# Optimization experiments

Hardware: AMD Instinct MI355X
Metric: run time of the kernel (lower is better)

The kernel has to match this reference:

```python
import jax, jax.numpy as jnp
import numpy as np

BN_EPS = 1e-5


def _interpolate(xyz1, xyz2, points2):
    # squared pairwise distances [B, N, S]
    d = (jnp.sum(xyz1 ** 2, -1)[:, :, None]
         + jnp.sum(xyz2 ** 2, -1)[:, None, :]
         - 2.0 * jnp.einsum('bnc,bsc->bns', xyz1, xyz2))
    # 3 smallest distances (torch does a full sort; top-3 is the same math)
    neg_d, idx = jax.lax.top_k(-d, 3)          # [B, N, 3]
    dists = -neg_d
    w = 1.0 / (dists + 1e-8)
    w = w / jnp.sum(w, -1, keepdims=True)
    # gather points2 features at idx: [B, N, 3, D]
    gathered = jnp.take_along_axis(points2[:, None, :, :],
                                   idx[:, :, :, None], axis=2)
    return jnp.sum(gathered * w[:, :, :, None], axis=2)  # [B, N, D]


def _conv_bn_relu(x, w, b, gamma, beta):
    # x: [B, N, Cin]; 1x1 Conv1d == per-point dense layer
    y = jnp.einsum('bnc,oc->bno', x, w) + b
    mean = jnp.mean(y, axis=(0, 1))
    var = jnp.mean((y - mean) ** 2, axis=(0, 1))  # biased var (torch BN training)
    y = (y - mean) * jax.lax.rsqrt(var + BN_EPS) * gamma + beta
    return jax.nn.relu(y)


def setup_inputs() -> dict:
    key = jax.random.key(0)
    ks = jax.random.split(key, 8)
    B, N, S, D1, D2 = 8, 8192, 2048, 128, 256
    in_ch, mlp = D1 + D2, [256, 128]
    inp = {
        'xyz1': jax.random.normal(ks[0], (B, N, 3), jnp.float32),
        'xyz2': jax.random.normal(ks[1], (B, S, 3), jnp.float32),
        'points1': jax.random.normal(ks[2], (B, N, D1), jnp.float32),
        'points2': jax.random.normal(ks[3], (B, S, D2), jnp.float32),
    }
    c = in_ch
    for i, o in enumerate(mlp):
        kw = jax.random.fold_in(ks[4], i)
        inp[f'w{i}'] = jax.random.normal(kw, (o, c), jnp.float32) * (1.0 / np.sqrt(c))
        inp[f'b{i}'] = jnp.zeros((o,), jnp.float32)
        inp[f'g{i}'] = jnp.ones((o,), jnp.float32)
        inp[f'beta{i}'] = jnp.zeros((o,), jnp.float32)
        c = o
    return inp


def reference(xyz1, xyz2, points1, points2,
              w0, b0, g0, beta0, w1, b1, g1, beta1):
    interp = _interpolate(xyz1, xyz2, points2)          # [B, N, D2]
    x = jnp.concatenate([points1, interp], axis=-1)     # [B, N, D1+D2]
    x = _conv_bn_relu(x, w0, b0, g0, beta0)
    x = _conv_bn_relu(x, w1, b1, g1, beta1)
    return x                                            # [B, N, mlp[-1]]
```

## Files before the change

### kernel.cpp

```cpp
#include <hip/hip_runtime.h>
#include <hip/hip_bf16.h>

#define BATCH 8
#define NPTS  8192
#define SPTS  2048
#define D1C   128
#define D2C   256
#define C_IN  384
#define O0    256
#define O1    128
#define MROWS (BATCH * NPTS)
#define NCHUNK 8
#define CHSZ   256

typedef __attribute__((ext_vector_type(8))) short short8v;
typedef __attribute__((ext_vector_type(4))) float f32x4;
typedef unsigned long long u64;

#define PKINIT 0x7FE0000000000000ULL

__device__ __forceinline__ unsigned short f2bf(float f) {
    union { float f; unsigned u; } v; v.f = f;
    unsigned u = v.u;
    return (unsigned short)((u + 0x7fffu + ((u >> 16) & 1u)) >> 16);
}
__device__ __forceinline__ float bf2f(unsigned short h) {
    union { unsigned u; float f; } v; v.u = ((unsigned)h) << 16;
    return v.f;
}
__device__ __forceinline__ void gload_lds16(const void* g, void* l) {
    __builtin_amdgcn_global_load_lds(
        (const __attribute__((address_space(1))) void*)g,
        (__attribute__((address_space(3))) void*)l, 16, 0, 0);
}

__device__ __forceinline__ double pack_di(float d, int idx) {
    union { float f; unsigned u; } b; b.f = d;
    unsigned db = b.u;
    unsigned u  = db ^ ((unsigned)((int)db >> 31) | 0x80000000u);
    union { u64 q; double x; } p;
    p.q = ((u64)u << 31) | (unsigned)idx;
    return p.x;
}
__device__ __forceinline__ void unpack_di(double x, float* d, int* idx) {
    union { double x; u64 q; } p; p.x = x;
    unsigned u = (unsigned)(p.q >> 31);
    unsigned db = (u & 0x80000000u) ? (u ^ 0x80000000u) : ~u;
    union { unsigned u; float f; } b; b.u = db;
    *d = b.f;
    *idx = (int)(p.q & 0x7FFu);
}
__device__ __forceinline__ void ins3(double& p0, double& p1, double& p2, double x) {
    double l0 = fmax(p0, x);
    p0 = fmin(p0, x);
    double l1 = fmax(p1, l0);
    p1 = fmin(p1, l0);
    p2 = fmin(p2, l1);
}

__global__ __launch_bounds__(256, 8) void nn3_scan(
    const float* __restrict__ xyz1, const float* __restrict__ xyz2,
    u64* __restrict__ candP)
{
    __shared__ float4 P[CHSZ];
    const int t  = threadIdx.x;
    const int qb = blockIdx.x;
    const int c  = blockIdx.y;
    const int b  = qb >> 5;

    {
        const float* src = xyz2 + ((size_t)b * SPTS + c * CHSZ) * 3;
        float px = src[t * 3 + 0];
        float py = src[t * 3 + 1];
        float pz = src[t * 3 + 2];
        P[t] = make_float4(px, py, pz, px * px + py * py + pz * pz);
    }
    __syncthreads();

    const int q = qb * 256 + t;
    const float* qp = xyz1 + (size_t)q * 3;
    const float qx = qp[0], qy = qp[1], qz = qp[2];
    const float qn = qx * qx + qy * qy + qz * qz;

    union { u64 q; double x; } init; init.q = PKINIT;
    double p0 = init.x, p1 = init.x, p2 = init.x;
    const int gbase = c * CHSZ;

    #pragma unroll 4
    for (int s = 0; s < CHSZ; ++s) {
        float4 p = P[s];
        float dot = qx * p.x + qy * p.y + qz * p.z;
        float d = (qn + p.w) - 2.0f * dot;
        ins3(p0, p1, p2, pack_di(d, gbase + s));
    }

    union { double x; u64 q; } o0, o1, o2;
    o0.x = p0; o1.x = p1; o2.x = p2;
    const size_t base = (size_t)c * (MROWS * 3) + (size_t)q * 3;
    candP[base + 0] = o0.q;
    candP[base + 1] = o1.q;
    candP[base + 2] = o2.q;
}

__global__ __launch_bounds__(256) void nn3_merge(
    const u64* __restrict__ candP,
    int* __restrict__ idx3, float* __restrict__ wgt3)
{
    const int q = blockIdx.x * 256 + threadIdx.x;

    union { u64 q; double x; } init; init.q = PKINIT;
    double p0 = init.x, p1 = init.x, p2 = init.x;

    #pragma unroll
    for (int c = 0; c < NCHUNK; ++c) {
        const size_t base = (size_t)c * (MROWS * 3) + (size_t)q * 3;
        #pragma unroll
        for (int j = 0; j < 3; ++j) {
            union { u64 q; double x; } v; v.q = candP[base + j];
            ins3(p0, p1, p2, v.x);
        }
    }

    float d0, d1, d2; int i0, i1, i2;
    unpack_di(p0, &d0, &i0);
    unpack_di(p1, &d1, &i1);
    unpack_di(p2, &d2, &i2);

    float wa = 1.0f / (d0 + 1e-8f);
    float wb = 1.0f / (d1 + 1e-8f);
    float wc = 1.0f / (d2 + 1e-8f);
    float inv = 1.0f / (wa + wb + wc);
    wa *= inv; wb *= inv; wc *= inv;

    idx3[q * 3 + 0] = i0;
    idx3[q * 3 + 1] = i1;
    idx3[q * 3 + 2] = i2;
    wgt3[q * 3 + 0] = wa;
    wgt3[q * 3 + 1] = wb;
    wgt3[q * 3 + 2] = wc;
}

__global__ __launch_bounds__(256) void cvt_weights(
    const float* __restrict__ w0, const float* __restrict__ w1,
    unsigned short* __restrict__ w0bf, unsigned short* __restrict__ w1bf)
{
    int i = blockIdx.x * 256 + threadIdx.x;
    const int n0 = O0 * C_IN / 4;
    const float* src; unsigned short* dst; int j;
    if (i < n0) { src = w0; dst = w0bf; j = i; }
    else        { src = w1; dst = w1bf; j = i - n0; }
    float4 v = ((const float4*)src)[j];
    ushort4 o;
    o.x = f2bf(v.x); o.y = f2bf(v.y); o.z = f2bf(v.z); o.w = f2bf(v.w);
    ((ushort4*)dst)[j] = o;
}

__global__ __launch_bounds__(256) void interp_kernel(
    const float* __restrict__ points2,
    const int* __restrict__ idx3, const float* __restrict__ wgt3,
    unsigned short* __restrict__ xI)
{
    const int w    = threadIdx.x >> 6;
    const int lane = threadIdx.x & 63;
    const int blk   = blockIdx.x;
    const int xcd   = blk & 7;
    const int local = blk >> 3;
    const int m     = (xcd * 2048 + local) * 4 + w;
    const int b     = xcd;

    const float* p2b = points2 + (size_t)b * SPTS * D2C;
    const int  gi0 = idx3[m * 3 + 0];
    const int  gi1 = idx3[m * 3 + 1];
    const int  gi2 = idx3[m * 3 + 2];
    const float w0 = wgt3[m * 3 + 0];
    const float w1 = wgt3[m * 3 + 1];
    const float w2 = wgt3[m * 3 + 2];

    float4 a  = *(const float4*)(p2b + (size_t)gi0 * D2C + lane * 4);
    float4 bb = *(const float4*)(p2b + (size_t)gi1 * D2C + lane * 4);
    float4 c  = *(const float4*)(p2b + (size_t)gi2 * D2C + lane * 4);

    ushort4 o;
    o.x = f2bf(w0 * a.x + w1 * bb.x + w2 * c.x);
    o.y = f2bf(w0 * a.y + w1 * bb.y + w2 * c.y);
    o.z = f2bf(w0 * a.z + w1 * bb.z + w2 * c.z);
    o.w = f2bf(w0 * a.w + w1 * bb.w + w2 * c.w);
    *(ushort4*)(xI + (size_t)m * D2C + lane * 4) = o;
}

__global__ __launch_bounds__(512, 4) void gemm0_mfma(
    const float* __restrict__ points1, const unsigned short* __restrict__ xI,
    const unsigned short* __restrict__ w0bf, const float* __restrict__ b0,
    unsigned short* __restrict__ y0bf,
    float* __restrict__ sum0, float* __restrict__ sq0)
{
    __shared__ __align__(16) unsigned short As[2][128 * 32];
    __shared__ __align__(16) unsigned short Bs[2][256 * 32];

    const int t    = threadIdx.x;
    const int lane = t & 63;
    const int w    = t >> 6;
    const int wm   = w >> 2;
    const int wn   = w & 3;
    const int rowBase = blockIdx.x * 128;

    const int r      = t >> 2;
    const int ks_log = (t & 3) ^ ((t >> 3) & 3);

    const float* p1row = points1 + (size_t)(rowBase + r) * D1C;
    const unsigned short* xrow = xI + (size_t)(rowBase + r) * D2C + ks_log * 8;
    const unsigned short* gB0 = w0bf + (size_t)r * C_IN + ks_log * 8;
    const unsigned short* gB1 = w0bf + (size_t)(128 + r) * C_IN + ks_log * 8;

    const int rp = (lane & 15) * 64 + (((lane >> 4) ^ ((lane >> 1) & 3)) * 16);

    f32x4 acc[4][4] = {};

    auto stage = [&](int buf, int kt) {
        gload_lds16(gB0 + kt * 32, (char*)Bs[buf] + w * 1024);
        gload_lds16(gB1 + kt * 32, (char*)Bs[buf] + 8192 + w * 1024);
        if (kt < 4) {
            const int k = kt * 32 + ks_log * 8;
            float4 f0 = *(const float4*)(p1row + k);
            float4 f1 = *(const float4*)(p1row + k + 4);
            short8v av;
            av[0] = (short)f2bf(f0.x); av[1] = (short)f2bf(f0.y);
            av[2] = (short)f2bf(f0.z); av[3] = (short)f2bf(f0.w);
            av[4] = (short)f2bf(f1.x); av[5] = (short)f2bf(f1.y);
            av[6] = (short)f2bf(f1.z); av[7] = (short)f2bf(f1.w);
            *(short8v*)(As[buf] + t * 8) = av;
        } else {
            gload_lds16(xrow + (kt - 4) * 32, (char*)As[buf] + w * 1024);
        }
    };

    auto compute = [&](int buf) {
        const char* aB = (const char*)As[buf] + (wm * 64) * 64 + rp;
        const char* bB = (const char*)Bs[buf] + (wn * 64) * 64 + rp;
        short8v a[4], bv[4];
        #pragma unroll
        for (int m = 0; m < 4; ++m) a[m]  = *(const short8v*)(aB + m * 1024);
        #pragma unroll
        for (int n = 0; n < 4; ++n) bv[n] = *(const short8v*)(bB + n * 1024);
        #pragma unroll
        for (int m = 0; m < 4; ++m)
            #pragma unroll
            for (int n = 0; n < 4; ++n)
                acc[m][n] = __builtin_amdgcn_mfma_f32_16x16x32_bf16(
                    a[m], bv[n], acc[m][n], 0, 0, 0);
    };

    stage(0, 0);
    __syncthreads();
    #pragma unroll
    for (int kt = 0; kt < C_IN / 32; ++kt) {
        if (kt + 1 < C_IN / 32) stage((kt + 1) & 1, kt + 1);
        compute(kt & 1);
        __syncthreads();
    }

    const int colw = wn * 64 + (lane & 15);
    const int rowE = rowBase + wm * 64 + ((lane >> 4) * 4);
    float bias[4];
    #pragma unroll
    for (int n = 0; n < 4; ++n) bias[n] = b0[colw + n * 16];

    float cs[4] = {0.f, 0.f, 0.f, 0.f}, cq[4] = {0.f, 0.f, 0.f, 0.f};
    #pragma unroll
    for (int m = 0; m < 4; ++m)
        #pragma unroll
        for (int n = 0; n < 4; ++n)
            #pragma unroll
            for (int j = 0; j < 4; ++j) {
                float v = acc[m][n][j] + bias[n];
                y0bf[(size_t)(rowE + m * 16 + j) * O0 + colw + n * 16] = f2bf(v);
                cs[n] += v; cq[n] += v * v;
            }

    #pragma unroll
    for (int n = 0; n < 4; ++n) {
        float s = cs[n], qv = cq[n];
        s  += __shfl_xor(s, 16);  s  += __shfl_xor(s, 32);
        qv += __shfl_xor(qv, 16); qv += __shfl_xor(qv, 32);
        if (lane < 16) {
            atomicAdd(&sum0[colw + n * 16], s);
            atomicAdd(&sq0[colw + n * 16], qv);
        }
    }
}

__global__ void stats_kernel(const float* __restrict__ sum, const float* __restrict__ sq,
                             const float* __restrict__ g, const float* __restrict__ beta,
                             float* __restrict__ scale, float* __restrict__ shift,
                             int C, float invM)
{
    int c = blockIdx.x * blockDim.x + threadIdx.x;
    if (c < C) {
        float mean = sum[c] * invM;
        float var  = sq[c] * invM - mean * mean;
        float s = g[c] * rsqrtf(var + 1e-5f);
        scale[c] = s;
        shift[c] = beta[c] - mean * s;
    }
}

__global__ __launch_bounds__(256, 2) void gemm1_mfma(
    const unsigned short* __restrict__ x1, const unsigned short* __restrict__ w1bf,
    const float* __restrict__ scale0, const float* __restrict__ shift0,
    const float* __restrict__ b1, unsigned short* __restrict__ y1bf,
    float* __restrict__ sum1, float* __restrict__ sq1)
{
    __shared__ __align__(16) unsigned short As[2][128 * 32];
    __shared__ __align__(16) unsigned short Bs[2][128 * 32];
    __shared__ float sc[O0], sh[O0];

    const int t    = threadIdx.x;
    const int lane = t & 63;
    const int w    = t >> 6;
    const int wm   = w >> 1, wn = w & 1;
    const int rowBase = blockIdx.x * 128;

    sc[t] = scale0[t];
    sh[t] = shift0[t];
    __syncthreads();

    const int r      = t >> 2;
    const int kl     = t & 3;
    const int kp     = kl ^ ((r >> 1) & 3);
    const int ks_log = kl ^ ((r >> 1) & 3);

    const unsigned short* gA0 = x1 + (size_t)(rowBase + r) * O0 + kl * 8;
    const unsigned short* gA1 = x1 + (size_t)(rowBase + 64 + r) * O0 + kl * 8;
    const unsigned short* gB0 = w1bf + (size_t)r * O0 + ks_log * 8;
    const unsigned short* gB1 = w1bf + (size_t)(64 + r) * O0 + ks_log * 8;

    const int rp = (lane & 15) * 64 + (((lane >> 4) ^ ((lane >> 1) & 3)) * 16);

    f32x4 acc[4][4] = {};

    auto stage = [&](int buf, int kt) {
        gload_lds16(gB0 + kt * 32, (char*)Bs[buf] + w * 1024);
        gload_lds16(gB1 + kt * 32, (char*)Bs[buf] + 4096 + w * 1024);

        const int ch = kt * 32 + kl * 8;
        float4 s0v = *(const float4*)(sc + ch);
        float4 s1v = *(const float4*)(sc + ch + 4);
        float4 h0v = *(const float4*)(sh + ch);
        float4 h1v = *(const float4*)(sh + ch + 4);
        short8v v0 = *(const short8v*)(gA0 + kt * 32);
        short8v v1 = *(const short8v*)(gA1 + kt * 32);
        short8v o0, o1;
        o0[0] = (short)f2bf(fmaxf(0.f, bf2f((unsigned short)v0[0]) * s0v.x + h0v.x));
        o0[1] = (short)f2bf(fmaxf(0.f, bf2f((unsigned short)v0[1]) * s0v.y + h0v.y));
        o0[2] = (short)f2bf(fmaxf(0.f, bf2f((unsigned short)v0[2]) * s0v.z + h0v.z));
        o0[3] = (short)f2bf(fmaxf(0.f, bf2f((unsigned short)v0[3]) * s0v.w + h0v.w));
        o0[4] = (short)f2bf(fmaxf(0.f, bf2f((unsigned short)v0[4]) * s1v.x + h1v.x));
        o0[5] = (short)f2bf(fmaxf(0.f, bf2f((unsigned short)v0[5]) * s1v.y + h1v.y));
        o0[6] = (short)f2bf(fmaxf(0.f, bf2f((unsigned short)v0[6]) * s1v.z + h1v.z));
        o0[7] = (short)f2bf(fmaxf(0.f, bf2f((unsigned short)v0[7]) * s1v.w + h1v.w));
        o1[0] = (short)f2bf(fmaxf(0.f, bf2f((unsigned short)v1[0]) * s0v.x + h0v.x));
        o1[1] = (short)f2bf(fmaxf(0.f, bf2f((unsigned short)v1[1]) * s0v.y + h0v.y));
        o1[2] = (short)f2bf(fmaxf(0.f, bf2f((unsigned short)v1[2]) * s0v.z + h0v.z));
        o1[3] = (short)f2bf(fmaxf(0.f, bf2f((unsigned short)v1[3]) * s0v.w + h0v.w));
        o1[4] = (short)f2bf(fmaxf(0.f, bf2f((unsigned short)v1[4]) * s1v.x + h1v.x));
        o1[5] = (short)f2bf(fmaxf(0.f, bf2f((unsigned short)v1[5]) * s1v.y + h1v.y));
        o1[6] = (short)f2bf(fmaxf(0.f, bf2f((unsigned short)v1[6]) * s1v.z + h1v.z));
        o1[7] = (short)f2bf(fmaxf(0.f, bf2f((unsigned short)v1[7]) * s1v.w + h1v.w));
        *(short8v*)(As[buf] + r * 32 + kp * 8) = o0;
        *(short8v*)(As[buf] + (64 + r) * 32 + kp * 8) = o1;
    };

    auto compute = [&](int buf) {
        const char* aB = (const char*)As[buf] + (wm * 64) * 64 + rp;
        const char* bB = (const char*)Bs[buf] + (wn * 64) * 64 + rp;
        short8v a[4], bv[4];
        #pragma unroll
        for (int m = 0; m < 4; ++m) a[m]  = *(const short8v*)(aB + m * 1024);
        #pragma unroll
        for (int n = 0; n < 4; ++n) bv[n] = *(const short8v*)(bB + n * 1024);
        #pragma unroll
        for (int m = 0; m < 4; ++m)
            #pragma unroll
            for (int n = 0; n < 4; ++n)
                acc[m][n] = __builtin_amdgcn_mfma_f32_16x16x32_bf16(
                    a[m], bv[n], acc[m][n], 0, 0, 0);
    };

    stage(0, 0);
    __syncthreads();
    #pragma unroll
    for (int kt = 0; kt < O0 / 32; ++kt) {
        if (kt + 1 < O0 / 32) stage((kt + 1) & 1, kt + 1);
        compute(kt & 1);
        __syncthreads();
    }

    const int colw = wn * 64 + (lane & 15);
    const int rowE = rowBase + wm * 64 + ((lane >> 4) * 4);
    float bias[4];
    #pragma unroll
    for (int n = 0; n < 4; ++n) bias[n] = b1[colw + n * 16];

    float cs[4] = {0.f, 0.f, 0.f, 0.f}, cq[4] = {0.f, 0.f, 0.f, 0.f};
    #pragma unroll
    for (int m = 0; m < 4; ++m)
        #pragma unroll
        for (int n = 0; n < 4; ++n)
            #pragma unroll
            for (int j = 0; j < 4; ++j) {
                float v = acc[m][n][j] + bias[n];
                y1bf[(size_t)(rowE + m * 16 + j) * O1 + colw + n * 16] = f2bf(v);
                cs[n] += v; cq[n] += v * v;
            }

    #pragma unroll
    for (int n = 0; n < 4; ++n) {
        float s = cs[n], qv = cq[n];
        s  += __shfl_xor(s, 16);  s  += __shfl_xor(s, 32);
        qv += __shfl_xor(qv, 16); qv += __shfl_xor(qv, 32);
        if (lane < 16) {
            atomicAdd(&sum1[colw + n * 16], s);
            atomicAdd(&sq1[colw + n * 16], qv);
        }
    }
}

__global__ __launch_bounds__(256) void bn_relu_out(
    const unsigned short* __restrict__ y1bf, float* __restrict__ out,
    const float* __restrict__ scale, const float* __restrict__ shift)
{
    int i = blockIdx.x * 256 + threadIdx.x;
    short8v v = ((const short8v*)y1bf)[i];
    int c = (i * 8) & (O1 - 1);
    float4 sa = *(const float4*)(scale + c);
    float4 sb = *(const float4*)(scale + c + 4);
    float4 ha = *(const float4*)(shift + c);
    float4 hb = *(const float4*)(shift + c + 4);
    float4 o0, o1;
    o0.x = fmaxf(0.f, bf2f((unsigned short)v[0]) * sa.x + ha.x);
    o0.y = fmaxf(0.f, bf2f((unsigned short)v[1]) * sa.y + ha.y);
    o0.z = fmaxf(0.f, bf2f((unsigned short)v[2]) * sa.z + ha.z);
    o0.w = fmaxf(0.f, bf2f((unsigned short)v[3]) * sa.w + ha.w);
    o1.x = fmaxf(0.f, bf2f((unsigned short)v[4]) * sb.x + hb.x);
    o1.y = fmaxf(0.f, bf2f((unsigned short)v[5]) * sb.y + hb.y);
    o1.z = fmaxf(0.f, bf2f((unsigned short)v[6]) * sb.z + hb.z);
    o1.w = fmaxf(0.f, bf2f((unsigned short)v[7]) * sb.w + hb.w);
    ((float4*)out)[i * 2 + 0] = o0;
    ((float4*)out)[i * 2 + 1] = o1;
}

extern "C" void kernel_launch(void* const* d_in, const int* in_sizes, int n_in,
                              void* d_out, int out_size, void* d_ws, size_t ws_size,
                              hipStream_t stream)
{
    const float* xyz1    = (const float*)d_in[0];
    const float* xyz2    = (const float*)d_in[1];
    const float* points1 = (const float*)d_in[2];
    const float* points2 = (const float*)d_in[3];
    const float* w0      = (const float*)d_in[4];
    const float* b0      = (const float*)d_in[5];
    const float* g0      = (const float*)d_in[6];
    const float* beta0   = (const float*)d_in[7];
    const float* w1      = (const float*)d_in[8];
    const float* b1      = (const float*)d_in[9];
    const float* g1      = (const float*)d_in[10];
    const float* beta1   = (const float*)d_in[11];

    float* wsf = (float*)d_ws;
    float* sum0   = wsf;
    float* sq0    = wsf + 256;
    float* sum1   = wsf + 512;
    float* sq1    = wsf + 640;
    float* scale0 = wsf + 768;
    float* shift0 = wsf + 1024;
    float* scale1 = wsf + 1280;
    float* shift1 = wsf + 1408;
    unsigned short* w0bf = (unsigned short*)(wsf + 1536);
    unsigned short* w1bf = (unsigned short*)(wsf + 50688);
    u64*    candP = (u64*)(wsf + 132608);
    int*    idx3  = (int*)(wsf + 3278336);
    float*  wgt3  = wsf + 3474944;
    unsigned short* y0bf = (unsigned short*)(wsf + 67072);
    unsigned short* xI   = (unsigned short*)(wsf + 8455680);
    unsigned short* y1bf = (unsigned short*)(wsf + 8455680);

    hipMemsetAsync(d_ws, 0, 768 * sizeof(float), stream);

    cvt_weights<<<(O0 * C_IN / 4 + O1 * O0 / 4) / 256, 256, 0, stream>>>(
        w0, w1, w0bf, w1bf);

    nn3_scan<<<dim3(MROWS / 256, NCHUNK), 256, 0, stream>>>(xyz1, xyz2, candP);
    nn3_merge<<<MROWS / 256, 256, 0, stream>>>(candP, idx3, wgt3);

    interp_kernel<<<MROWS / 4, 256, 0, stream>>>(points2, idx3, wgt3, xI);

    gemm0_mfma<<<MROWS / 128, 512, 0, stream>>>(
        points1, xI, w0bf, b0, y0bf, sum0, sq0);

    stats_kernel<<<1, 256, 0, stream>>>(sum0, sq0, g0, beta0, scale0, shift0,
                                        O0, 1.0f / MROWS);

    gemm1_mfma<<<MROWS / 128, 256, 0, stream>>>(
        y0bf, w1bf, scale0, shift0, b1, y1bf, sum1, sq1);

    stats_kernel<<<1, 128, 0, stream>>>(sum1, sq1, g1, beta1, scale1, shift1,
                                        O1, 1.0f / MROWS);

    bn_relu_out<<<(MROWS * O1 / 8) / 256, 256, 0, stream>>>(
        y1bf, (float*)d_out, scale1, shift1);
}
```

Before: 187.2 us.

## Register-block four queries per thread in NN3 scan with float med3 top-3

```diff
diff --git a/kernel.cpp b/kernel.cpp
--- a/kernel.cpp
+++ b/kernel.cpp
@@ -10,8 +10,8 @@
 #define O0    256
 #define O1    128
 #define MROWS (BATCH * NPTS)
-#define NCHUNK 8
-#define CHSZ   256
+#define NCH   16
+#define CH2   128
 
 typedef __attribute__((ext_vector_type(8))) short short8v;
 typedef __attribute__((ext_vector_type(4))) float f32x4;
@@ -34,13 +34,11 @@
         (__attribute__((address_space(3))) void*)l, 16, 0, 0);
 }
 
-__device__ __forceinline__ double pack_di(float d, int idx) {
+__device__ __forceinline__ u64 pack_di(float d, int idx) {
     union { float f; unsigned u; } b; b.f = d;
     unsigned db = b.u;
     unsigned u  = db ^ ((unsigned)((int)db >> 31) | 0x80000000u);
-    union { u64 q; double x; } p;
-    p.q = ((u64)u << 31) | (unsigned)idx;
-    return p.x;
+    return ((u64)u << 31) | (unsigned)idx;
 }
 __device__ __forceinline__ void unpack_di(double x, float* d, int* idx) {
     union { double x; u64 q; } p; p.x = x;
@@ -58,18 +56,18 @@
     p2 = fmin(p2, l1);
 }
 
-__global__ __launch_bounds__(256, 8) void nn3_scan(
+__global__ __launch_bounds__(256, 2) void nn3_scan4(
     const float* __restrict__ xyz1, const float* __restrict__ xyz2,
     u64* __restrict__ candP)
 {
-    __shared__ float4 P[CHSZ];
+    __shared__ float4 P[CH2];
     const int t  = threadIdx.x;
     const int qb = blockIdx.x;
     const int c  = blockIdx.y;
-    const int b  = qb >> 5;
-
-    {
-        const float* src = xyz2 + ((size_t)b * SPTS + c * CHSZ) * 3;
+    const int b  = qb >> 3;
+
+    if (t < CH2) {
+        const float* src = xyz2 + ((size_t)b * SPTS + c * CH2) * 3;
         float px = src[t * 3 + 0];
         float py = src[t * 3 + 1];
         float pz = src[t * 3 + 2];
@@ -77,29 +75,49 @@
     }
     __syncthreads();
 
-    const int q = qb * 256 + t;
-    const float* qp = xyz1 + (size_t)q * 3;
-    const float qx = qp[0], qy = qp[1], qz = qp[2];
-    const float qn = qx * qx + qy * qy + qz * qz;
-
-    union { u64 q; double x; } init; init.q = PKINIT;
-    double p0 = init.x, p1 = init.x, p2 = init.x;
-    const int gbase = c * CHSZ;
-
-    #pragma unroll 4
-    for (int s = 0; s < CHSZ; ++s) {
+    const int q0 = qb * 1024 + t;
+    float qx[4], qy[4], qz[4], qn[4];
+    #pragma unroll
+    for (int k = 0; k < 4; ++k) {
+        const float* qp = xyz1 + (size_t)(q0 + k * 256) * 3;
+        qx[k] = qp[0]; qy[k] = qp[1]; qz[k] = qp[2];
+        qn[k] = qx[k] * qx[k] + qy[k] * qy[k] + qz[k] * qz[k];
+    }
+
+    float d0[4], d1[4], d2[4];
+    int   i0[4], i1[4], i2[4];
+    #pragma unroll
+    for (int k = 0; k < 4; ++k) {
+        d0[k] = 1e30f; d1[k] = 1e30f; d2[k] = 1e30f;
+        i0[k] = 0;     i1[k] = 0;     i2[k] = 0;
+    }
+    const int gbase = c * CH2;
+
+    #pragma unroll 2
+    for (int s = 0; s < CH2; ++s) {
         float4 p = P[s];
-        float dot = qx * p.x + qy * p.y + qz * p.z;
-        float d = (qn + p.w) - 2.0f * dot;
-        ins3(p0, p1, p2, pack_di(d, gbase + s));
-    }
-
-    union { double x; u64 q; } o0, o1, o2;
-    o0.x = p0; o1.x = p1; o2.x = p2;
-    const size_t base = (size_t)c * (MROWS * 3) + (size_t)q * 3;
-    candP[base + 0] = o0.q;
-    candP[base + 1] = o1.q;
-    candP[base + 2] = o2.q;
+        const int gi = gbase + s;
+        #pragma unroll
+        for (int k = 0; k < 4; ++k) {
+            float dot = qx[k] * p.x + qy[k] * p.y + qz[k] * p.z;
+            float d = (qn[k] + p.w) - 2.0f * dot;
+            bool c0 = d < d0[k], c1 = d < d1[k], c2 = d < d2[k];
+            float t2 = __builtin_amdgcn_fmed3f(d, d1[k], d2[k]);
+            float t1 = __builtin_amdgcn_fmed3f(d, d0[k], d1[k]);
+            i2[k] = c1 ? i1[k] : (c2 ? gi : i2[k]);
+            i1[k] = c0 ? i0[k] : (c1 ? gi : i1[k]);
+            i0[k] = c0 ? gi : i0[k];
+            d2[k] = t2; d1[k] = t1; d0[k] = fminf(d, d0[k]);
+        }
+    }
+
+    #pragma unroll
+    for (int k = 0; k < 4; ++k) {
+        const size_t base = (size_t)c * (MROWS * 3) + (size_t)(q0 + k * 256) * 3;
+        candP[base + 0] = pack_di(d0[k], i0[k]);
+        candP[base + 1] = pack_di(d1[k], i1[k]);
+        candP[base + 2] = pack_di(d2[k], i2[k]);
+    }
 }
 
 __global__ __launch_bounds__(256) void nn3_merge(
@@ -112,7 +130,7 @@
     double p0 = init.x, p1 = init.x, p2 = init.x;
 
     #pragma unroll
-    for (int c = 0; c < NCHUNK; ++c) {
+    for (int c = 0; c < NCH; ++c) {
         const size_t base = (size_t)c * (MROWS * 3) + (size_t)q * 3;
         #pragma unroll
         for (int j = 0; j < 3; ++j) {
@@ -478,8 +496,8 @@
     unsigned short* w0bf = (unsigned short*)(wsf + 1536);
     unsigned short* w1bf = (unsigned short*)(wsf + 50688);
     u64*    candP = (u64*)(wsf + 132608);
-    int*    idx3  = (int*)(wsf + 3278336);
-    float*  wgt3  = wsf + 3474944;
+    int*    idx3  = (int*)(wsf + 6424064);
+    float*  wgt3  = wsf + 6620672;
     unsigned short* y0bf = (unsigned short*)(wsf + 67072);
     unsigned short* xI   = (unsigned short*)(wsf + 8455680);
     unsigned short* y1bf = (unsigned short*)(wsf + 8455680);
@@ -489,7 +507,7 @@
     cvt_weights<<<(O0 * C_IN / 4 + O1 * O0 / 4) / 256, 256, 0, stream>>>(
         w0, w1, w0bf, w1bf);
 
-    nn3_scan<<<dim3(MROWS / 256, NCHUNK), 256, 0, stream>>>(xyz1, xyz2, candP);
+    nn3_scan4<<<dim3(MROWS / 1024, NCH), 256, 0, stream>>>(xyz1, xyz2, candP);
     nn3_merge<<<MROWS / 256, 256, 0, stream>>>(candP, idx3, wgt3);
 
     interp_kernel<<<MROWS / 4, 256, 0, stream>>>(points2, idx3, wgt3, xI);
```

Result: slower. 205.5 us (+9.8%).
